# Kernel tuning notes

Hardware: AMD Instinct MI355X
Metric: run time of the kernel (lower is better)

The kernel has to match this reference:

```python
import jax, jax.numpy as jnp
import numpy as np

N = 100_000   # total nodes across all subgraphs in batch
E = 1_600_000 # edges (avg degree 16)
B = 1_000     # number of subgraphs
D = 128       # in_dim = out_dim
SZ = N // B   # nodes per subgraph


def setup_inputs() -> dict:
    key = jax.random.key(0)
    ks = jax.random.split(key, 8)
    feat = jax.random.normal(ks[0], (N, D), dtype=jnp.float32)
    edge_src = jax.random.randint(ks[1], (E,), 0, N, dtype=jnp.int32)
    edge_dst = jax.random.randint(ks[2], (E,), 0, N, dtype=jnp.int32)
    # pre-normalized edge weights (is_normed=True path)
    edge_w = jax.random.uniform(ks[3], (E,), dtype=jnp.float32)
    s = 1.0 / np.sqrt(D)
    W1 = jax.random.normal(ks[4], (D, D), dtype=jnp.float32) * s
    W2 = jax.random.normal(ks[5], (D, D), dtype=jnp.float32) * s
    Wp = jax.random.normal(ks[6], (D, D), dtype=jnp.float32) * s
    b1 = jnp.zeros((D,), jnp.float32)
    b2 = jnp.zeros((D,), jnp.float32)
    bp = jnp.zeros((D,), jnp.float32)
    # contiguous equal-size subgraphs; target = first node of each subgraph
    seg_ids = jnp.repeat(jnp.arange(B, dtype=jnp.int32), SZ)
    target = jnp.arange(B, dtype=jnp.int32) * SZ
    size_subg = jnp.full((B,), float(SZ), jnp.float32)
    return dict(feat=feat, edge_w=edge_w, W1=W1, b1=b1, W2=W2, b2=b2,
                Wp=Wp, bp=bp, size_subg=size_subg,
                edge_src=edge_src, edge_dst=edge_dst,
                seg_ids=seg_ids, target=target)


def _gcn_layer(x, src, dst, w, W, b):
    # sparse A_hat @ x : gather src features, weight, scatter-add into dst
    msg = x[src] * w[:, None]                       # [E, D]
    agg = jax.ops.segment_sum(msg, dst, num_segments=N)  # [N, D]
    return jax.nn.relu(agg @ W + b)


def reference(feat, edge_w, W1, b1, W2, b2, Wp, bp, size_subg,
              edge_src, edge_dst, seg_ids, target):
    # two stacked GCN layers (self.structure = [structure1, structure2])
    h1 = _gcn_layer(feat, edge_src, edge_dst, edge_w, W1, b1)
    h2 = _gcn_layer(h1, edge_src, edge_dst, edge_w, W2, b2)
    # ResPool: residual-sum over layer outputs, mean pool per subgraph,
    # add target-node embedding (residual), then linear + relu
    h = h1 + h2                                              # [N, D]
    pooled = jax.ops.segment_sum(h, seg_ids, num_segments=B)
    pooled = pooled / size_subg[:, None] + h[target]         # [B, D]
    emb = jax.nn.relu(pooled @ Wp + bp)
    # F.normalize(p=2, dim=1), eps=1e-12
    norm = jnp.sqrt(jnp.sum(emb * emb, axis=1, keepdims=True))
    emb = emb / jnp.maximum(norm, 1e-12)
    return emb  # EnsembleDummy just returns the single branch
```

## Files before the change

### kernel.cpp

```cpp
#include <hip/hip_runtime.h>

#define DD 128
#define CHUNK 4096
#define BSH 8
#define MAXBK 512
#define MAXCH 512
#define CAP 6144
#define CAPN 48

typedef _Float16 half8 __attribute__((ext_vector_type(8)));
typedef _Float16 half4v __attribute__((ext_vector_type(4)));
typedef float floatx4 __attribute__((ext_vector_type(4)));
typedef float floatx2 __attribute__((ext_vector_type(2)));

__global__ __launch_bounds__(256) void k_prep(const float* __restrict__ W1,
                                              _Float16* __restrict__ W1t,
                                              const float* __restrict__ W2,
                                              _Float16* __restrict__ W2t) {
    int idx = blockIdx.x * 256 + threadIdx.x;
    const float* W = (idx < DD * DD) ? W1 : W2;
    _Float16* Wt = (idx < DD * DD) ? W1t : W2t;
    int id = idx & (DD * DD - 1);
    int n = id >> 7, k = id & 127;
    Wt[n * DD + k] = (_Float16)W[k * DD + n];
}

__global__ __launch_bounds__(512) void k_histg1(const int* __restrict__ dst,
                                                int* __restrict__ histT,
                                                int E, int nChunks,
                                                const float* __restrict__ A,
                                                const _Float16* __restrict__ Wt,
                                                unsigned char* __restrict__ Y, int nrows) {
    if (blockIdx.x < nChunks) {
        __shared__ int lhist[MAXBK];
        int tid = threadIdx.x;
        lhist[tid] = 0;
        __syncthreads();
        int beg = blockIdx.x * CHUNK;
        int end = min(beg + CHUNK, E);
        for (int k = beg + tid; k < end; k += 512)
            atomicAdd(&lhist[dst[k] >> BSH], 1);
        __syncthreads();
        histT[tid * MAXCH + blockIdx.x] = lhist[tid];
    } else {
        int gblk = blockIdx.x - nChunks;
        int wave = threadIdx.x >> 6;
        int lane = threadIdx.x & 63;
        int row0 = gblk * 256 + wave * 32;
        int m = lane & 15;
        int q = lane >> 4;
        int r0 = min(row0 + m, nrows - 1);
        int r1 = min(row0 + 16 + m, nrows - 1);

        floatx4 acc[2][8];
        #pragma unroll
        for (int t = 0; t < 2; ++t)
            #pragma unroll
            for (int c = 0; c < 8; ++c)
                acc[t][c] = (floatx4){0.f, 0.f, 0.f, 0.f};

        #pragma unroll
        for (int ks = 0; ks < 4; ++ks) {
            int kbase = ks * 32 + q * 8;
            float4 x0 = *reinterpret_cast<const float4*>(A + (size_t)r0 * DD + kbase);
            float4 x1 = *reinterpret_cast<const float4*>(A + (size_t)r0 * DD + kbase + 4);
            float4 y0 = *reinterpret_cast<const float4*>(A + (size_t)r1 * DD + kbase);
            float4 y1 = *reinterpret_cast<const float4*>(A + (size_t)r1 * DD + kbase + 4);
            half8 a0, a1;
            a0[0]=(_Float16)x0.x; a0[1]=(_Float16)x0.y; a0[2]=(_Float16)x0.z; a0[3]=(_Float16)x0.w;
            a0[4]=(_Float16)x1.x; a0[5]=(_Float16)x1.y; a0[6]=(_Float16)x1.z; a0[7]=(_Float16)x1.w;
            a1[0]=(_Float16)y0.x; a1[1]=(_Float16)y0.y; a1[2]=(_Float16)y0.z; a1[3]=(_Float16)y0.w;
            a1[4]=(_Float16)y1.x; a1[5]=(_Float16)y1.y; a1[6]=(_Float16)y1.z; a1[7]=(_Float16)y1.w;
            #pragma unroll
            for (int c = 0; c < 8; ++c) {
                half8 b = *reinterpret_cast<const half8*>(Wt + (size_t)(c * 16 + m) * DD + kbase);
                acc[0][c] = __builtin_amdgcn_mfma_f32_16x16x32_f16(b, a0, acc[0][c], 0, 0, 0);
                acc[1][c] = __builtin_amdgcn_mfma_f32_16x16x32_f16(b, a1, acc[1][c], 0, 0, 0);
            }
        }

        #pragma unroll
        for (int t = 0; t < 2; ++t) {
            int row = row0 + t * 16 + m;
            if (row >= nrows) continue;
            size_t rb = (size_t)row * DD;
            #pragma unroll
            for (int c = 0; c < 8; ++c) {
                int col = c * 16 + q * 4;
                int u = 0;
                u = __builtin_amdgcn_cvt_pk_fp8_f32(acc[t][c][0], acc[t][c][1], u, false);
                u = __builtin_amdgcn_cvt_pk_fp8_f32(acc[t][c][2], acc[t][c][3], u, true);
                *reinterpret_cast<unsigned int*>(&Y[rb + col]) = (unsigned int)u;
            }
        }
    }
}

__global__ __launch_bounds__(512) void k_scan(int* __restrict__ histT,
                                              int* __restrict__ gcur, int nChunks) {
    __shared__ int wsum[8];
    int b = blockIdx.x;
    int c = threadIdx.x;
    int v = (c < nChunks) ? histT[b * MAXCH + c] : 0;
    int lane = c & 63, wave = c >> 6;
    int inc = v;
    #pragma unroll
    for (int off = 1; off < 64; off <<= 1) {
        int t = __shfl_up(inc, off, 64);
        if (lane >= off) inc += t;
    }
    if (lane == 63) wsum[wave] = inc;
    __syncthreads();
    if (c == 0) {
        int run = 0;
        #pragma unroll
        for (int j = 0; j < 8; ++j) { int t = wsum[j]; wsum[j] = run; run += t; }
    }
    __syncthreads();
    int ex = inc - v + wsum[wave];
    if (c < nChunks) histT[b * MAXCH + c] = ex;
    if (c == nChunks - 1) gcur[b] = ex + v;
}

__global__ __launch_bounds__(512) void k_pass1(const int* __restrict__ src,
                                               const int* __restrict__ dst,
                                               const float* __restrict__ w,
                                               const int* __restrict__ histT,
                                               int2* __restrict__ out, int E, int NB) {
    __shared__ int2 stg[CHUNK];
    __shared__ unsigned short bok[CHUNK];
    __shared__ int lhist[MAXBK];
    __shared__ int loff[MAXBK];
    __shared__ int lbase[MAXBK];
    __shared__ int lcur[MAXBK];
    int tid = threadIdx.x;
    lhist[tid] = 0;
    __syncthreads();

    int beg = blockIdx.x * CHUNK;
    int end = min(beg + CHUNK, E);
    for (int k = beg + tid; k < end; k += 512)
        atomicAdd(&lhist[dst[k] >> BSH], 1);
    __syncthreads();
    if (tid < 64) {
        int base = tid * 8, v[8], s = 0;
        #pragma unroll
        for (int j = 0; j < 8; ++j) { v[j] = lhist[base + j]; s += v[j]; }
        int scn = s;
        #pragma unroll
        for (int off = 1; off < 64; off <<= 1) {
            int t = __shfl_up(scn, off, 64);
            if (tid >= off) scn += t;
        }
        int ex = scn - s;
        #pragma unroll
        for (int j = 0; j < 8; ++j) { loff[base + j] = ex; lcur[base + j] = ex; ex += v[j]; }
    }
    __syncthreads();
    if (tid < NB)
        lbase[tid] = tid * CAP + histT[tid * MAXCH + blockIdx.x];
    for (int k = beg + tid; k < end; k += 512) {
        int d = dst[k];
        int b = d >> BSH;
        int p = atomicAdd(&lcur[b], 1);
        stg[p] = make_int2(src[k] | ((d & ((1 << BSH) - 1)) << 17),
                           __float_as_int(w[k]));
        bok[p] = (unsigned short)b;
    }
    __syncthreads();
    int total = end - beg;
    for (int j = tid; j < total; j += 512) {
        int b = bok[j];
        out[lbase[b] + (j - loff[b])] = stg[j];
    }
}

__global__ __launch_bounds__(512) void k_pass2(const int2* __restrict__ bkt,
                                               const int* __restrict__ gcur,
                                               int* __restrict__ cnt,
                                               int2* __restrict__ edges, int N) {
    __shared__ int lhist[1 << BSH];
    __shared__ int loff[1 << BSH];
    __shared__ int lcur[1 << BSH];
    int tid = threadIdx.x;
    int b = blockIdx.x;
    int base = b * CAP;
    int nrec = gcur[b];
    int d0 = b << BSH;

    if (tid < (1 << BSH)) lhist[tid] = 0;
    __syncthreads();
    for (int i = tid; i < nrec; i += 512)
        atomicAdd(&lhist[(unsigned)bkt[base + i].x >> 17], 1);
    __syncthreads();
    if (tid < 64) {
        int bs = tid * 4, vv[4], s = 0;
        #pragma unroll
        for (int j = 0; j < 4; ++j) { vv[j] = lhist[bs + j]; s += vv[j]; }
        int scn = s;
        #pragma unroll
        for (int off = 1; off < 64; off <<= 1) {
            int t = __shfl_up(scn, off, 64);
            if (tid >= off) scn += t;
        }
        int ex = scn - s;
        #pragma unroll
        for (int j = 0; j < 4; ++j) {
            loff[bs + j] = ex; lcur[bs + j] = ex; ex += vv[j];
        }
    }
    __syncthreads();
    if (tid < (1 << BSH)) {
        int d = d0 + tid;
        if (d < N)
            cnt[d] = min(lhist[tid], CAPN);
    }
    for (int i = tid; i < nrec; i += 512) {
        int2 r = bkt[base + i];
        int dl = (unsigned)r.x >> 17;
        int slot = atomicAdd(&lcur[dl], 1) - loff[dl];
        if (slot < CAPN)
            edges[(size_t)(d0 + dl) * CAPN + slot] = make_int2(r.x & 0x1FFFF, r.y);
    }
}

__global__ __launch_bounds__(256) void k_gemm_f16A(const _Float16* __restrict__ A,
                                                   const _Float16* __restrict__ Wt,
                                                   unsigned char* __restrict__ Y,
                                                   int nrows) {
    int wave = threadIdx.x >> 6;
    int lane = threadIdx.x & 63;
    int row0 = blockIdx.x * 128 + wave * 32;
    int m = lane & 15;
    int q = lane >> 4;

    floatx4 acc[2][8];
    #pragma unroll
    for (int t = 0; t < 2; ++t)
        #pragma unroll
        for (int c = 0; c < 8; ++c)
            acc[t][c] = (floatx4){0.f, 0.f, 0.f, 0.f};

    #pragma unroll
    for (int ks = 0; ks < 4; ++ks) {
        int kbase = ks * 32 + q * 8;
        half8 a0 = *reinterpret_cast<const half8*>(A + (size_t)(row0 + m) * DD + kbase);
        half8 a1 = *reinterpret_cast<const half8*>(A + (size_t)(row0 + 16 + m) * DD + kbase);
        #pragma unroll
        for (int c = 0; c < 8; ++c) {
            half8 b = *reinterpret_cast<const half8*>(Wt + (size_t)(c * 16 + m) * DD + kbase);
            acc[0][c] = __builtin_amdgcn_mfma_f32_16x16x32_f16(b, a0, acc[0][c], 0, 0, 0);
            acc[1][c] = __builtin_amdgcn_mfma_f32_16x16x32_f16(b, a1, acc[1][c], 0, 0, 0);
        }
    }

    #pragma unroll
    for (int t = 0; t < 2; ++t) {
        int row = row0 + t * 16 + m;
        if (row >= nrows) continue;
        size_t rb = (size_t)row * DD;
        #pragma unroll
        for (int c = 0; c < 8; ++c) {
            int col = c * 16 + q * 4;
            int u = 0;
            u = __builtin_amdgcn_cvt_pk_fp8_f32(acc[t][c][0], acc[t][c][1], u, false);
            u = __builtin_amdgcn_cvt_pk_fp8_f32(acc[t][c][2], acc[t][c][3], u, true);
            *reinterpret_cast<unsigned int*>(&Y[rb + col]) = (unsigned int)u;
        }
    }
}

__global__ __launch_bounds__(256) void k_agg_eplg(const unsigned char* __restrict__ x,
                                                  const int* __restrict__ cnt,
                                                  const int2* __restrict__ edges,
                                                  const float* __restrict__ bias,
                                                  const _Float16* __restrict__ resid,
                                                  _Float16* __restrict__ out, int N) {
    int gwave = (blockIdx.x * blockDim.x + threadIdx.x) >> 6;
    int lane = threadIdx.x & 63;
    int half = lane >> 5;
    int hl = lane & 31;
    int wid = gwave * 2 + half;
    if (wid >= N) return;
    int g = hl >> 3;
    int sl = hl & 7;
    int c = cnt[wid];
    int beg = wid * CAPN;
    floatx2 acc2[8];
    #pragma unroll
    for (int j = 0; j < 8; ++j) acc2[j] = (floatx2){0.f, 0.f};

    int2 e[8];
    #pragma unroll
    for (int u = 0; u < 8; ++u) e[u] = edges[beg + u * 4 + g];
    uint4 v[8];
    #pragma unroll
    for (int u = 0; u < 8; ++u) {
        int row = min(max(e[u].x, 0), N - 1);
        v[u] = *reinterpret_cast<const uint4*>(x + (size_t)row * DD + sl * 16);
    }
    int end = min(c, CAPN);
    #pragma unroll
    for (int u = 0; u < 8; ++u) {
        float wv = (u * 4 + g < end) ? __int_as_float(e[u].y) : 0.f;
        floatx2 w2 = (floatx2){wv, wv};
        acc2[0] += __builtin_amdgcn_cvt_pk_f32_fp8((int)v[u].x, false) * w2;
        acc2[1] += __builtin_amdgcn_cvt_pk_f32_fp8((int)v[u].x, true)  * w2;
        acc2[2] += __builtin_amdgcn_cvt_pk_f32_fp8((int)v[u].y, false) * w2;
        acc2[3] += __builtin_amdgcn_cvt_pk_f32_fp8((int)v[u].y, true)  * w2;
        acc2[4] += __builtin_amdgcn_cvt_pk_f32_fp8((int)v[u].z, false) * w2;
        acc2[5] += __builtin_amdgcn_cvt_pk_f32_fp8((int)v[u].z, true)  * w2;
        acc2[6] += __builtin_amdgcn_cvt_pk_f32_fp8((int)v[u].w, false) * w2;
        acc2[7] += __builtin_amdgcn_cvt_pk_f32_fp8((int)v[u].w, true)  * w2;
    }
    if (end > 32) {
        int2 e2[4];
        #pragma unroll
        for (int u = 0; u < 4; ++u) e2[u] = edges[beg + 32 + u * 4 + g];
        uint4 v2[4];
        #pragma unroll
        for (int u = 0; u < 4; ++u) {
            int row = min(max(e2[u].x, 0), N - 1);
            v2[u] = *reinterpret_cast<const uint4*>(x + (size_t)row * DD + sl * 16);
        }
        #pragma unroll
        for (int u = 0; u < 4; ++u) {
            float wv = (32 + u * 4 + g < end) ? __int_as_float(e2[u].y) : 0.f;
            floatx2 w2 = (floatx2){wv, wv};
            acc2[0] += __builtin_amdgcn_cvt_pk_f32_fp8((int)v2[u].x, false) * w2;
            acc2[1] += __builtin_amdgcn_cvt_pk_f32_fp8((int)v2[u].x, true)  * w2;
            acc2[2] += __builtin_amdgcn_cvt_pk_f32_fp8((int)v2[u].y, false) * w2;
            acc2[3] += __builtin_amdgcn_cvt_pk_f32_fp8((int)v2[u].y, true)  * w2;
            acc2[4] += __builtin_amdgcn_cvt_pk_f32_fp8((int)v2[u].z, false) * w2;
            acc2[5] += __builtin_amdgcn_cvt_pk_f32_fp8((int)v2[u].z, true)  * w2;
            acc2[6] += __builtin_amdgcn_cvt_pk_f32_fp8((int)v2[u].w, false) * w2;
            acc2[7] += __builtin_amdgcn_cvt_pk_f32_fp8((int)v2[u].w, true)  * w2;
        }
    }

    #pragma unroll
    for (int j = 0; j < 8; ++j) {
        acc2[j][0] += __shfl_xor(acc2[j][0], 8, 64);
        acc2[j][1] += __shfl_xor(acc2[j][1], 8, 64);
        acc2[j][0] += __shfl_xor(acc2[j][0], 16, 64);
        acc2[j][1] += __shfl_xor(acc2[j][1], 16, 64);
    }
    if (g == 0) {
        float acc[16];
        #pragma unroll
        for (int j = 0; j < 8; ++j) { acc[2 * j] = acc2[j][0]; acc[2 * j + 1] = acc2[j][1]; }
        size_t rb = (size_t)wid * DD + sl * 16;
        float bb[16];
        #pragma unroll
        for (int q = 0; q < 4; ++q) {
            float4 b4 = *reinterpret_cast<const float4*>(&bias[sl * 16 + q * 4]);
            bb[q * 4 + 0] = b4.x; bb[q * 4 + 1] = b4.y;
            bb[q * 4 + 2] = b4.z; bb[q * 4 + 3] = b4.w;
        }
        half8 o0, o1;
        if (resid) {
            half8 r0 = *reinterpret_cast<const half8*>(&resid[rb]);
            half8 r1 = *reinterpret_cast<const half8*>(&resid[rb + 8]);
            #pragma unroll
            for (int j = 0; j < 8; ++j) {
                float v = acc[j] + bb[j];
                v = v > 0.f ? v : 0.f;
                o0[j] = (_Float16)(v + (float)r0[j]);
            }
            #pragma unroll
            for (int j = 0; j < 8; ++j) {
                float v = acc[8 + j] + bb[8 + j];
                v = v > 0.f ? v : 0.f;
                o1[j] = (_Float16)(v + (float)r1[j]);
            }
        } else {
            #pragma unroll
            for (int j = 0; j < 8; ++j) {
                float v = acc[j] + bb[j];
                o0[j] = (_Float16)(v > 0.f ? v : 0.f);
            }
            #pragma unroll
            for (int j = 0; j < 8; ++j) {
                float v = acc[8 + j] + bb[8 + j];
                o1[j] = (_Float16)(v > 0.f ? v : 0.f);
            }
        }
        *reinterpret_cast<half8*>(&out[rb]) = o0;
        *reinterpret_cast<half8*>(&out[rb + 8]) = o1;
    }
}

__global__ __launch_bounds__(256) void k_pool_final(const _Float16* __restrict__ h,
                                                    const int* __restrict__ target,
                                                    const float* __restrict__ size_subg,
                                                    const float* __restrict__ Wp,
                                                    const float* __restrict__ bp,
                                                    float* __restrict__ out, int SZ) {
    __shared__ float part[16][DD];
    __shared__ float p[DD];
    __shared__ float wsum[2];
    int b = blockIdx.x;
    int t = threadIdx.x;
    int c = t & 15;
    int r = t >> 4;
    const _Float16* hp = h + (size_t)b * SZ * DD;
    float s[8] = {0.f, 0.f, 0.f, 0.f, 0.f, 0.f, 0.f, 0.f};
    for (int n = r; n < SZ; n += 16) {
        half8 v = *reinterpret_cast<const half8*>(hp + (size_t)n * DD + c * 8);
        #pragma unroll
        for (int j = 0; j < 8; ++j) s[j] += (float)v[j];
    }
    #pragma unroll
    for (int j = 0; j < 8; ++j) part[r][c * 8 + j] = s[j];
    __syncthreads();
    if (t < DD) {
        float sum = 0.f;
        #pragma unroll
        for (int rr = 0; rr < 16; ++rr) sum += part[rr][t];
        int tg = target[b];
        p[t] = sum / size_subg[b] + (float)h[(size_t)tg * DD + t];
    }
    __syncthreads();
    if (t < DD) {
        float acc = 0.f;
        #pragma unroll 4
        for (int k = 0; k < DD; ++k) acc = fmaf(p[k], Wp[k * DD + t], acc);
        float e = acc + bp[t];
        e = e > 0.f ? e : 0.f;
        float sq = e * e;
        #pragma unroll
        for (int off = 32; off > 0; off >>= 1) sq += __shfl_down(sq, off, 64);
        int lane = t & 63, w = t >> 6;
        if (lane == 0) wsum[w] = sq;
        __syncthreads();
        float norm = sqrtf(wsum[0] + wsum[1]);
        float scale = 1.f / fmaxf(norm, 1e-12f);
        out[b * DD + t] = e * scale;
    } else {
        __syncthreads();
    }
}

extern "C" void kernel_launch(void* const* d_in, const int* in_sizes, int n_in,
                              void* d_out, int out_size, void* d_ws, size_t ws_size,
                              hipStream_t stream) {
    const float* feat      = (const float*)d_in[0];
    const float* edge_w    = (const float*)d_in[1];
    const float* W1        = (const float*)d_in[2];
    const float* b1        = (const float*)d_in[3];
    const float* W2        = (const float*)d_in[4];
    const float* b2        = (const float*)d_in[5];
    const float* Wp        = (const float*)d_in[6];
    const float* bp        = (const float*)d_in[7];
    const float* size_subg = (const float*)d_in[8];
    const int*   edge_src  = (const int*)d_in[9];
    const int*   edge_dst  = (const int*)d_in[10];
    const int*   target    = (const int*)d_in[12];

    const int N  = in_sizes[0] / DD;
    const int E  = in_sizes[1];
    const int B  = in_sizes[8];
    const int SZ = N / B;

    const int P  = ((N + 127) / 128) * 128;
    const int NB = (N + (1 << BSH) - 1) >> BSH;
    const int nChunks = (E + CHUNK - 1) / CHUNK;

    char* ws = (char*)d_ws;
    size_t off = 0;
    auto alloc = [&](size_t bytes) {
        void* p = ws + off;
        off += (bytes + 255) & ~(size_t)255;
        return p;
    };
    unsigned char* Y = (unsigned char*)alloc((size_t)P * DD);
    _Float16* h1     = (_Float16*)alloc((size_t)P * DD * 2);
    _Float16* H      = (_Float16*)alloc((size_t)P * DD * 2);
    _Float16* W1t    = (_Float16*)alloc((size_t)DD * DD * 2);
    _Float16* W2t    = (_Float16*)alloc((size_t)DD * DD * 2);
    int*   cnt       = (int*)alloc((size_t)N * 4);
    int*   gcur      = (int*)alloc((size_t)MAXBK * 4);
    int*   histT     = (int*)alloc((size_t)MAXBK * MAXCH * 4);
    int2*  edges_bkt = (int2*)alloc((size_t)NB * CAP * 8);
    int2*  edges     = (int2*)alloc((size_t)N * CAPN * 8);

    k_prep<<<128, 256, 0, stream>>>(W1, W1t, W2, W2t);

    int g1Blocks = (N + 255) / 256;
    k_histg1<<<nChunks + g1Blocks, 512, 0, stream>>>(
        edge_dst, histT, E, nChunks, feat, W1t, Y, N);

    k_scan<<<NB, 512, 0, stream>>>(histT, gcur, nChunks);

    k_pass1<<<nChunks, 512, 0, stream>>>(edge_src, edge_dst, edge_w, histT,
                                         edges_bkt, E, NB);

    k_pass2<<<NB, 512, 0, stream>>>(edges_bkt, gcur, cnt, edges, N);

    int nodePairs  = (N + 1) / 2;
    int aggBlocks  = (nodePairs * 64 + 255) / 256;
    int gemmBlocks = (N + 127) / 128;

    k_agg_eplg<<<aggBlocks, 256, 0, stream>>>(Y, cnt, edges, b1, nullptr, h1, N);
    k_gemm_f16A<<<gemmBlocks, 256, 0, stream>>>(h1, W2t, Y, N);
    k_agg_eplg<<<aggBlocks, 256, 0, stream>>>(Y, cnt, edges, b2, h1, H, N);
    k_pool_final<<<B, 256, 0, stream>>>(H, target, size_subg, Wp, bp,
                                        (float*)d_out, SZ);
}
```

Measured before the change: 302.7 us.

## Regroup kernel fusions: merge weight prep into scan, layer-1 GEMM into pass2

```diff
diff --git a/kernel.cpp b/kernel.cpp
--- a/kernel.cpp
+++ b/kernel.cpp
@@ -13,113 +13,60 @@
 typedef float floatx4 __attribute__((ext_vector_type(4)));
 typedef float floatx2 __attribute__((ext_vector_type(2)));
 
-__global__ __launch_bounds__(256) void k_prep(const float* __restrict__ W1,
-                                              _Float16* __restrict__ W1t,
-                                              const float* __restrict__ W2,
-                                              _Float16* __restrict__ W2t) {
-    int idx = blockIdx.x * 256 + threadIdx.x;
-    const float* W = (idx < DD * DD) ? W1 : W2;
-    _Float16* Wt = (idx < DD * DD) ? W1t : W2t;
-    int id = idx & (DD * DD - 1);
-    int n = id >> 7, k = id & 127;
-    Wt[n * DD + k] = (_Float16)W[k * DD + n];
-}
-
-__global__ __launch_bounds__(512) void k_histg1(const int* __restrict__ dst,
-                                                int* __restrict__ histT,
-                                                int E, int nChunks,
-                                                const float* __restrict__ A,
-                                                const _Float16* __restrict__ Wt,
-                                                unsigned char* __restrict__ Y, int nrows) {
-    if (blockIdx.x < nChunks) {
-        __shared__ int lhist[MAXBK];
-        int tid = threadIdx.x;
-        lhist[tid] = 0;
-        __syncthreads();
-        int beg = blockIdx.x * CHUNK;
-        int end = min(beg + CHUNK, E);
-        for (int k = beg + tid; k < end; k += 512)
-            atomicAdd(&lhist[dst[k] >> BSH], 1);
-        __syncthreads();
-        histT[tid * MAXCH + blockIdx.x] = lhist[tid];
+__global__ __launch_bounds__(512) void k_hist(const int* __restrict__ dst,
+                                              int* __restrict__ histT, int E) {
+    __shared__ int lhist[MAXBK];
+    int tid = threadIdx.x;
+    lhist[tid] = 0;
+    __syncthreads();
+    int beg = blockIdx.x * CHUNK;
+    int end = min(beg + CHUNK, E);
+    for (int k = beg + tid; k < end; k += 512)
+        atomicAdd(&lhist[dst[k] >> BSH], 1);
+    __syncthreads();
+    histT[tid * MAXCH + blockIdx.x] = lhist[tid];
+}
+
+__global__ __launch_bounds__(512) void k_scanprep(int* __restrict__ histT,
+                                                  int* __restrict__ gcur, int nChunks,
+                                                  int NB,
+                                                  const float* __restrict__ W1,
+                                                  _Float16* __restrict__ W1t,
+                                                  const float* __restrict__ W2,
+                                                  _Float16* __restrict__ W2t) {
+    if (blockIdx.x < NB) {
+        __shared__ int wsum[8];
+        int b = blockIdx.x;
+        int c = threadIdx.x;
+        int v = (c < nChunks) ? histT[b * MAXCH + c] : 0;
+        int lane = c & 63, wave = c >> 6;
+        int inc = v;
+        #pragma unroll
+        for (int off = 1; off < 64; off <<= 1) {
+            int t = __shfl_up(inc, off, 64);
+            if (lane >= off) inc += t;
+        }
+        if (lane == 63) wsum[wave] = inc;
+        __syncthreads();
+        if (c == 0) {
+            int run = 0;
+            #pragma unroll
+            for (int j = 0; j < 8; ++j) { int t = wsum[j]; wsum[j] = run; run += t; }
+        }
+        __syncthreads();
+        int ex = inc - v + wsum[wave];
+        if (c < nChunks) histT[b * MAXCH + c] = ex;
+        if (c == nChunks - 1) gcur[b] = ex + v;
     } else {
-        int gblk = blockIdx.x - nChunks;
-        int wave = threadIdx.x >> 6;
-        int lane = threadIdx.x & 63;
-        int row0 = gblk * 256 + wave * 32;
-        int m = lane & 15;
-        int q = lane >> 4;
-        int r0 = min(row0 + m, nrows - 1);
-        int r1 = min(row0 + 16 + m, nrows - 1);
-
-        floatx4 acc[2][8];
-        #pragma unroll
-        for (int t = 0; t < 2; ++t)
-            #pragma unroll
-            for (int c = 0; c < 8; ++c)
-                acc[t][c] = (floatx4){0.f, 0.f, 0.f, 0.f};
-
-        #pragma unroll
-        for (int ks = 0; ks < 4; ++ks) {
-            int kbase = ks * 32 + q * 8;
-            float4 x0 = *reinterpret_cast<const float4*>(A + (size_t)r0 * DD + kbase);
-            float4 x1 = *reinterpret_cast<const float4*>(A + (size_t)r0 * DD + kbase + 4);
-            float4 y0 = *reinterpret_cast<const float4*>(A + (size_t)r1 * DD + kbase);
-            float4 y1 = *reinterpret_cast<const float4*>(A + (size_t)r1 * DD + kbase + 4);
-            half8 a0, a1;
-            a0[0]=(_Float16)x0.x; a0[1]=(_Float16)x0.y; a0[2]=(_Float16)x0.z; a0[3]=(_Float16)x0.w;
-            a0[4]=(_Float16)x1.x; a0[5]=(_Float16)x1.y; a0[6]=(_Float16)x1.z; a0[7]=(_Float16)x1.w;
-            a1[0]=(_Float16)y0.x; a1[1]=(_Float16)y0.y; a1[2]=(_Float16)y0.z; a1[3]=(_Float16)y0.w;
-            a1[4]=(_Float16)y1.x; a1[5]=(_Float16)y1.y; a1[6]=(_Float16)y1.z; a1[7]=(_Float16)y1.w;
-            #pragma unroll
-            for (int c = 0; c < 8; ++c) {
-                half8 b = *reinterpret_cast<const half8*>(Wt + (size_t)(c * 16 + m) * DD + kbase);
-                acc[0][c] = __builtin_amdgcn_mfma_f32_16x16x32_f16(b, a0, acc[0][c], 0, 0, 0);
-                acc[1][c] = __builtin_amdgcn_mfma_f32_16x16x32_f16(b, a1, acc[1][c], 0, 0, 0);
-            }
-        }
-
-        #pragma unroll
-        for (int t = 0; t < 2; ++t) {
-            int row = row0 + t * 16 + m;
-            if (row >= nrows) continue;
-            size_t rb = (size_t)row * DD;
-            #pragma unroll
-            for (int c = 0; c < 8; ++c) {
-                int col = c * 16 + q * 4;
-                int u = 0;
-                u = __builtin_amdgcn_cvt_pk_fp8_f32(acc[t][c][0], acc[t][c][1], u, false);
-                u = __builtin_amdgcn_cvt_pk_fp8_f32(acc[t][c][2], acc[t][c][3], u, true);
-                *reinterpret_cast<unsigned int*>(&Y[rb + col]) = (unsigned int)u;
-            }
-        }
-    }
-}
-
-__global__ __launch_bounds__(512) void k_scan(int* __restrict__ histT,
-                                              int* __restrict__ gcur, int nChunks) {
-    __shared__ int wsum[8];
-    int b = blockIdx.x;
-    int c = threadIdx.x;
-    int v = (c < nChunks) ? histT[b * MAXCH + c] : 0;
-    int lane = c & 63, wave = c >> 6;
-    int inc = v;
-    #pragma unroll
-    for (int off = 1; off < 64; off <<= 1) {
-        int t = __shfl_up(inc, off, 64);
-        if (lane >= off) inc += t;
-    }
-    if (lane == 63) wsum[wave] = inc;
-    __syncthreads();
-    if (c == 0) {
-        int run = 0;
-        #pragma unroll
-        for (int j = 0; j < 8; ++j) { int t = wsum[j]; wsum[j] = run; run += t; }
-    }
-    __syncthreads();
-    int ex = inc - v + wsum[wave];
-    if (c < nChunks) histT[b * MAXCH + c] = ex;
-    if (c == nChunks - 1) gcur[b] = ex + v;
+        int idx = (blockIdx.x - NB) * 512 + threadIdx.x;
+        if (idx < 2 * DD * DD) {
+            const float* W = (idx < DD * DD) ? W1 : W2;
+            _Float16* Wt = (idx < DD * DD) ? W1t : W2t;
+            int id = idx & (DD * DD - 1);
+            int n = id >> 7, k = id & 127;
+            Wt[n * DD + k] = (_Float16)W[k * DD + n];
+        }
+    }
 }
 
 __global__ __launch_bounds__(512) void k_pass1(const int* __restrict__ src,
@@ -175,52 +122,108 @@
     }
 }
 
-__global__ __launch_bounds__(512) void k_pass2(const int2* __restrict__ bkt,
-                                               const int* __restrict__ gcur,
-                                               int* __restrict__ cnt,
-                                               int2* __restrict__ edges, int N) {
-    __shared__ int lhist[1 << BSH];
-    __shared__ int loff[1 << BSH];
-    __shared__ int lcur[1 << BSH];
-    int tid = threadIdx.x;
-    int b = blockIdx.x;
-    int base = b * CAP;
-    int nrec = gcur[b];
-    int d0 = b << BSH;
-
-    if (tid < (1 << BSH)) lhist[tid] = 0;
-    __syncthreads();
-    for (int i = tid; i < nrec; i += 512)
-        atomicAdd(&lhist[(unsigned)bkt[base + i].x >> 17], 1);
-    __syncthreads();
-    if (tid < 64) {
-        int bs = tid * 4, vv[4], s = 0;
-        #pragma unroll
-        for (int j = 0; j < 4; ++j) { vv[j] = lhist[bs + j]; s += vv[j]; }
-        int scn = s;
-        #pragma unroll
-        for (int off = 1; off < 64; off <<= 1) {
-            int t = __shfl_up(scn, off, 64);
-            if (tid >= off) scn += t;
-        }
-        int ex = scn - s;
-        #pragma unroll
-        for (int j = 0; j < 4; ++j) {
-            loff[bs + j] = ex; lcur[bs + j] = ex; ex += vv[j];
-        }
-    }
-    __syncthreads();
-    if (tid < (1 << BSH)) {
-        int d = d0 + tid;
-        if (d < N)
-            cnt[d] = min(lhist[tid], CAPN);
-    }
-    for (int i = tid; i < nrec; i += 512) {
-        int2 r = bkt[base + i];
-        int dl = (unsigned)r.x >> 17;
-        int slot = atomicAdd(&lcur[dl], 1) - loff[dl];
-        if (slot < CAPN)
-            edges[(size_t)(d0 + dl) * CAPN + slot] = make_int2(r.x & 0x1FFFF, r.y);
+__global__ __launch_bounds__(512) void k_p2g1(const int2* __restrict__ bkt,
+                                              const int* __restrict__ gcur,
+                                              int* __restrict__ cnt,
+                                              int2* __restrict__ edges, int N, int NB,
+                                              const float* __restrict__ A,
+                                              const _Float16* __restrict__ Wt,
+                                              unsigned char* __restrict__ Y, int nrows) {
+    if (blockIdx.x < NB) {
+        __shared__ int lhist[1 << BSH];
+        __shared__ int loff[1 << BSH];
+        __shared__ int lcur[1 << BSH];
+        int tid = threadIdx.x;
+        int b = blockIdx.x;
+        int base = b * CAP;
+        int nrec = gcur[b];
+        int d0 = b << BSH;
+
+        if (tid < (1 << BSH)) lhist[tid] = 0;
+        __syncthreads();
+        for (int i = tid; i < nrec; i += 512)
+            atomicAdd(&lhist[(unsigned)bkt[base + i].x >> 17], 1);
+        __syncthreads();
+        if (tid < 64) {
+            int bs = tid * 4, vv[4], s = 0;
+            #pragma unroll
+            for (int j = 0; j < 4; ++j) { vv[j] = lhist[bs + j]; s += vv[j]; }
+            int scn = s;
+            #pragma unroll
+            for (int off = 1; off < 64; off <<= 1) {
+                int t = __shfl_up(scn, off, 64);
+                if (tid >= off) scn += t;
+            }
+            int ex = scn - s;
+            #pragma unroll
+            for (int j = 0; j < 4; ++j) {
+                loff[bs + j] = ex; lcur[bs + j] = ex; ex += vv[j];
+            }
+        }
+        __syncthreads();
+        if (tid < (1 << BSH)) {
+            int d = d0 + tid;
+            if (d < N)
+                cnt[d] = min(lhist[tid], CAPN);
+        }
+        for (int i = tid; i < nrec; i += 512) {
+            int2 r = bkt[base + i];
+            int dl = (unsigned)r.x >> 17;
+            int slot = atomicAdd(&lcur[dl], 1) - loff[dl];
+            if (slot < CAPN)
+                edges[(size_t)(d0 + dl) * CAPN + slot] = make_int2(r.x & 0x1FFFF, r.y);
+        }
+    } else {
+        int gblk = blockIdx.x - NB;
+        int wave = threadIdx.x >> 6;
+        int lane = threadIdx.x & 63;
+        int row0 = gblk * 256 + wave * 32;
+        int m = lane & 15;
+        int q = lane >> 4;
+        int r0 = min(row0 + m, nrows - 1);
+        int r1 = min(row0 + 16 + m, nrows - 1);
+
+        floatx4 acc[2][8];
+        #pragma unroll
+        for (int t = 0; t < 2; ++t)
+            #pragma unroll
+            for (int c = 0; c < 8; ++c)
+                acc[t][c] = (floatx4){0.f, 0.f, 0.f, 0.f};
+
+        #pragma unroll
+        for (int ks = 0; ks < 4; ++ks) {
+            int kbase = ks * 32 + q * 8;
+            float4 x0 = *reinterpret_cast<const float4*>(A + (size_t)r0 * DD + kbase);
+            float4 x1 = *reinterpret_cast<const float4*>(A + (size_t)r0 * DD + kbase + 4);
+            float4 y0 = *reinterpret_cast<const float4*>(A + (size_t)r1 * DD + kbase);
+            float4 y1 = *reinterpret_cast<const float4*>(A + (size_t)r1 * DD + kbase + 4);
+            half8 a0, a1;
+            a0[0]=(_Float16)x0.x; a0[1]=(_Float16)x0.y; a0[2]=(_Float16)x0.z; a0[3]=(_Float16)x0.w;
+            a0[4]=(_Float16)x1.x; a0[5]=(_Float16)x1.y; a0[6]=(_Float16)x1.z; a0[7]=(_Float16)x1.w;
+            a1[0]=(_Float16)y0.x; a1[1]=(_Float16)y0.y; a1[2]=(_Float16)y0.z; a1[3]=(_Float16)y0.w;
+            a1[4]=(_Float16)y1.x; a1[5]=(_Float16)y1.y; a1[6]=(_Float16)y1.z; a1[7]=(_Float16)y1.w;
+            #pragma unroll
+            for (int c = 0; c < 8; ++c) {
+                half8 b = *reinterpret_cast<const half8*>(Wt + (size_t)(c * 16 + m) * DD + kbase);
+                acc[0][c] = __builtin_amdgcn_mfma_f32_16x16x32_f16(b, a0, acc[0][c], 0, 0, 0);
+                acc[1][c] = __builtin_amdgcn_mfma_f32_16x16x32_f16(b, a1, acc[1][c], 0, 0, 0);
+            }
+        }
+
+        #pragma unroll
+        for (int t = 0; t < 2; ++t) {
+            int row = row0 + t * 16 + m;
+            if (row >= nrows) continue;
+            size_t rb = (size_t)row * DD;
+            #pragma unroll
+            for (int c = 0; c < 8; ++c) {
+                int col = c * 16 + q * 4;
+                int u = 0;
+                u = __builtin_amdgcn_cvt_pk_fp8_f32(acc[t][c][0], acc[t][c][1], u, false);
+                u = __builtin_amdgcn_cvt_pk_fp8_f32(acc[t][c][2], acc[t][c][3], u, true);
+                *reinterpret_cast<unsigned int*>(&Y[rb + col]) = (unsigned int)u;
+            }
+        }
     }
 }
 
@@ -484,18 +487,18 @@
     int2*  edges_bkt = (int2*)alloc((size_t)NB * CAP * 8);
     int2*  edges     = (int2*)alloc((size_t)N * CAPN * 8);
 
-    k_prep<<<128, 256, 0, stream>>>(W1, W1t, W2, W2t);
-
-    int g1Blocks = (N + 255) / 256;
-    k_histg1<<<nChunks + g1Blocks, 512, 0, stream>>>(
-        edge_dst, histT, E, nChunks, feat, W1t, Y, N);
-
-    k_scan<<<NB, 512, 0, stream>>>(histT, gcur, nChunks);
+    k_hist<<<nChunks, 512, 0, stream>>>(edge_dst, histT, E);
+
+    int prepBlocks = (2 * DD * DD + 511) / 512;
+    k_scanprep<<<NB + prepBlocks, 512, 0, stream>>>(histT, gcur, nChunks, NB,
+                                                    W1, W1t, W2, W2t);
 
     k_pass1<<<nChunks, 512, 0, stream>>>(edge_src, edge_dst, edge_w, histT,
                                          edges_bkt, E, NB);
 
-    k_pass2<<<NB, 512, 0, stream>>>(edges_bkt, gcur, cnt, edges, N);
+    int g1Blocks = (N + 255) / 256;
+    k_p2g1<<<NB + g1Blocks, 512, 0, stream>>>(edges_bkt, gcur, cnt, edges, N, NB,
+                                              feat, W1t, Y, N);
 
     int nodePairs  = (N + 1) / 2;
     int aggBlocks  = (nodePairs * 64 + 255) / 256;
```

After: 300.8 us. No clear change (-0.6%).
